# Performance work log

Hardware: AMD Instinct MI355X
Metric: run time of the kernel (lower is better)

## Reference

```python
import jax, jax.numpy as jnp
import numpy as np

B, S, D = 4, 4096, 64
D_MODEL = 64


def setup_inputs() -> dict:
    key = jax.random.key(0)
    kq, kk, kv, km = jax.random.split(key, 4)
    q = jax.random.normal(kq, (B, S, D), dtype=jnp.float32)
    k = jax.random.normal(kk, (B, S, D), dtype=jnp.float32)
    v = jax.random.normal(kv, (B, S, D), dtype=jnp.float32)
    mask = jax.random.uniform(km, (B, S, S), dtype=jnp.float32)
    return {"q": q, "k": k, "v": v, "mask": mask}


def reference(q, k, v, mask):
    dk = jnp.sqrt(jnp.asarray(D_MODEL, dtype=q.dtype))
    # [B,S,S] scores; multiplicative (non-additive) mask applied pre-softmax
    scaled_qk = jnp.einsum('bqd,bkd->bqk', q, k) / dk
    scaled_qk = scaled_qk * mask
    attn = jax.nn.softmax(scaled_qk, axis=-1)
    return jnp.einsum('bqk,bkd->bqd', attn, v)
```

## Files before the change

### kernel.cpp

```cpp
#include <hip/hip_runtime.h>
#include <hip/hip_bf16.h>

#define S_LEN 4096
#define DH 64
#define NBATCH 4

typedef __attribute__((ext_vector_type(8))) short short8;
typedef __attribute__((ext_vector_type(4))) float f32x4;


__global__ __launch_bounds__(256) void cvt_qk_kernel(const float* __restrict__ q,
                                                     const float* __restrict__ k,
                                                     __hip_bfloat16* __restrict__ qb,
                                                     __hip_bfloat16* __restrict__ kb) {
  int i = blockIdx.x * 256 + threadIdx.x;
  qb[i] = __float2bfloat16(q[i]);
  kb[i] = __float2bfloat16(k[i]);
}

__global__ __launch_bounds__(256) void cvt_vT_kernel(const float* __restrict__ v,
                                                     __hip_bfloat16* __restrict__ vt) {
  int i = blockIdx.x * 256 + threadIdx.x;
  int d = i & (DH - 1);
  int s = (i >> 6) & (S_LEN - 1);
  int b = i >> 18;
  vt[(((size_t)b * DH + d) << 12) + s] = __float2bfloat16(v[i]);
}


__global__ __launch_bounds__(256, 4) void fa_kernel(
    const __hip_bfloat16* __restrict__ qb, const __hip_bfloat16* __restrict__ kb,
    const __hip_bfloat16* __restrict__ vt, const float* __restrict__ mask,
    float* __restrict__ out) {
  __shared__ __align__(16) __hip_bfloat16 lds_p[4][16][40];
  __shared__ float lds_O[4][16][64];
  __shared__ float lds_l[4][16];

  const int tid = threadIdx.x;
  const int w = tid >> 6;
  const int lane = tid & 63;
  const int quad = lane >> 4;
  const int n16 = lane & 15;

  const int b = blockIdx.x >> 8;
  const int q0 = (blockIdx.x & 255) << 4;

  const __hip_bfloat16* qrow = qb + (size_t)(b * S_LEN + q0 + n16) * DH;
  const short8 aQ0 = *(const short8*)(qrow + quad * 8);
  const short8 aQ1 = *(const short8*)(qrow + 32 + quad * 8);

  f32x4 O0 = {0.f, 0.f, 0.f, 0.f}, O1 = O0, O2 = O0, O3 = O0;
  float lacc[4] = {0.f, 0.f, 0.f, 0.f};

  const float* mrows[4];
#pragma unroll
  for (int r = 0; r < 4; ++r)
    mrows[r] = mask + ((size_t)b * S_LEN + q0 + quad * 4 + r) * S_LEN;

  const int kstart = w * (S_LEN / 4);
  const __hip_bfloat16* vbase = vt + ((size_t)(b * DH) << 12);

  for (int it = 0; it < (S_LEN / 4) / 32; ++it) {
    const int k0 = kstart + it * 32;

    const __hip_bfloat16* kr0 = kb + (size_t)(b * S_LEN + k0 + n16) * DH;
    const short8 b00 = *(const short8*)(kr0 + quad * 8);
    const short8 b01 = *(const short8*)(kr0 + 32 + quad * 8);
    const short8 b10 = *(const short8*)(kr0 + 16 * DH + quad * 8);
    const short8 b11 = *(const short8*)(kr0 + 16 * DH + 32 + quad * 8);

    const f32x4 z = {0.f, 0.f, 0.f, 0.f};
    f32x4 s0 = __builtin_amdgcn_mfma_f32_16x16x32_bf16(aQ0, b00, z, 0, 0, 0);
    s0 = __builtin_amdgcn_mfma_f32_16x16x32_bf16(aQ1, b01, s0, 0, 0, 0);
    f32x4 s1 = __builtin_amdgcn_mfma_f32_16x16x32_bf16(aQ0, b10, z, 0, 0, 0);
    s1 = __builtin_amdgcn_mfma_f32_16x16x32_bf16(aQ1, b11, s1, 0, 0, 0);

#pragma unroll
    for (int r = 0; r < 4; ++r) {
      float p0 = __expf(s0[r] * 0.125f * mrows[r][k0 + n16]);
      float p1 = __expf(s1[r] * 0.125f * mrows[r][k0 + 16 + n16]);
      lacc[r] += p0 + p1;
      lds_p[w][quad * 4 + r][n16] = __float2bfloat16(p0);
      lds_p[w][quad * 4 + r][16 + n16] = __float2bfloat16(p1);
    }

    const short8 aP = *(const short8*)(&lds_p[w][n16][quad * 8]);

    const __hip_bfloat16* vp = vbase + k0 + quad * 8 + ((size_t)n16 << 12);
    const short8 v0 = *(const short8*)(vp);
    const short8 v1 = *(const short8*)(vp + ((size_t)16 << 12));
    const short8 v2 = *(const short8*)(vp + ((size_t)32 << 12));
    const short8 v3 = *(const short8*)(vp + ((size_t)48 << 12));

    O0 = __builtin_amdgcn_mfma_f32_16x16x32_bf16(aP, v0, O0, 0, 0, 0);
    O1 = __builtin_amdgcn_mfma_f32_16x16x32_bf16(aP, v1, O1, 0, 0, 0);
    O2 = __builtin_amdgcn_mfma_f32_16x16x32_bf16(aP, v2, O2, 0, 0, 0);
    O3 = __builtin_amdgcn_mfma_f32_16x16x32_bf16(aP, v3, O3, 0, 0, 0);
  }

#pragma unroll
  for (int r = 0; r < 4; ++r) {
#pragma unroll
    for (int off = 1; off < 16; off <<= 1) lacc[r] += __shfl_xor(lacc[r], off);
  }

#pragma unroll
  for (int r = 0; r < 4; ++r) {
    int row = quad * 4 + r;
    lds_O[w][row][n16] = O0[r];
    lds_O[w][row][16 + n16] = O1[r];
    lds_O[w][row][32 + n16] = O2[r];
    lds_O[w][row][48 + n16] = O3[r];
    if (n16 == 0) lds_l[w][row] = lacc[r];
  }
  __syncthreads();

  const int r = tid >> 4;
  const int c = (tid & 15) << 2;
  const float linv =
      1.0f / (lds_l[0][r] + lds_l[1][r] + lds_l[2][r] + lds_l[3][r]);
  f32x4 o;
#pragma unroll
  for (int j = 0; j < 4; ++j)
    o[j] = (lds_O[0][r][c + j] + lds_O[1][r][c + j] + lds_O[2][r][c + j] +
            lds_O[3][r][c + j]) *
           linv;
  *(f32x4*)(out + (size_t)(b * S_LEN + q0 + r) * DH + c) = o;
}

extern "C" void kernel_launch(void* const* d_in, const int* in_sizes, int n_in,
                              void* d_out, int out_size, void* d_ws, size_t ws_size,
                              hipStream_t stream) {
  const float* q = (const float*)d_in[0];
  const float* k = (const float*)d_in[1];
  const float* v = (const float*)d_in[2];
  const float* mask = (const float*)d_in[3];
  float* out = (float*)d_out;

  __hip_bfloat16* qb = (__hip_bfloat16*)d_ws;
  __hip_bfloat16* kb = qb + (size_t)NBATCH * S_LEN * DH;
  __hip_bfloat16* vt = kb + (size_t)NBATCH * S_LEN * DH;

  const int nconv_blocks = (NBATCH * S_LEN * DH) / 256;
  cvt_qk_kernel<<<nconv_blocks, 256, 0, stream>>>(q, k, qb, kb);
  cvt_vT_kernel<<<nconv_blocks, 256, 0, stream>>>(v, vt);
  fa_kernel<<<NBATCH * (S_LEN / 16), 256, 0, stream>>>(qb, kb, vt, mask, out);
}
```

Measured before the change: 475.0 us.

## Prefetch mask and K two iterations ahead, interleave warp key ranges, vectorize conversions

The attention kernel now software-pipelines the mask and K fragment loads, using a double-buffered register prefetch that runs two iterations ahead. It also changes the key assignment so the four warps interleave 32-key chunks instead of each owning a contiguous quarter. The Q/K conversion kernel is vectorized to four elements per thread, and the V transpose now goes through a padded LDS tile so that reads and writes are coalesced. These changes aim to hide the latency of the dominant mask stream and to cut prep-kernel overhead, at the cost of more registers per thread.

```diff
diff --git a/kernel.cpp b/kernel.cpp
--- a/kernel.cpp
+++ b/kernel.cpp
@@ -5,34 +5,63 @@
 #define DH 64
 #define NBATCH 4
 
-typedef __attribute__((ext_vector_type(8))) short short8;
+typedef __attribute__((ext_vector_type(8))) short bf16x8;
+typedef __attribute__((ext_vector_type(4))) short bf16x4;
 typedef __attribute__((ext_vector_type(4))) float f32x4;
 
+static __device__ __forceinline__ short f2bf(float x) {
+  __hip_bfloat16 h = __float2bfloat16(x);
+  return *reinterpret_cast<short*>(&h);
+}
+
+#define MFMA(a, b, c) __builtin_amdgcn_mfma_f32_16x16x32_bf16((a), (b), (c), 0, 0, 0)
 
 __global__ __launch_bounds__(256) void cvt_qk_kernel(const float* __restrict__ q,
                                                      const float* __restrict__ k,
-                                                     __hip_bfloat16* __restrict__ qb,
-                                                     __hip_bfloat16* __restrict__ kb) {
-  int i = blockIdx.x * 256 + threadIdx.x;
-  qb[i] = __float2bfloat16(q[i]);
-  kb[i] = __float2bfloat16(k[i]);
+                                                     short* __restrict__ qb,
+                                                     short* __restrict__ kb) {
+  int i = (blockIdx.x * 256 + threadIdx.x) * 4;
+  f32x4 xq = *(const f32x4*)(q + i);
+  f32x4 xk = *(const f32x4*)(k + i);
+  bf16x4 oq, ok;
+#pragma unroll
+  for (int j = 0; j < 4; ++j) { oq[j] = f2bf(xq[j]); ok[j] = f2bf(xk[j]); }
+  *(bf16x4*)(qb + i) = oq;
+  *(bf16x4*)(kb + i) = ok;
 }
 
 __global__ __launch_bounds__(256) void cvt_vT_kernel(const float* __restrict__ v,
-                                                     __hip_bfloat16* __restrict__ vt) {
-  int i = blockIdx.x * 256 + threadIdx.x;
-  int d = i & (DH - 1);
-  int s = (i >> 6) & (S_LEN - 1);
-  int b = i >> 18;
-  vt[(((size_t)b * DH + d) << 12) + s] = __float2bfloat16(v[i]);
+                                                     short* __restrict__ vt) {
+  __shared__ float tile[64][65];
+  const int t = threadIdx.x;
+  const int b = blockIdx.x >> 6;
+  const int s0 = (blockIdx.x & 63) << 6;
+#pragma unroll
+  for (int p = 0; p < 4; ++p) {
+    const int r = p * 16 + (t >> 4);
+    const int c = (t & 15) * 4;
+    const f32x4 x = *(const f32x4*)(v + (size_t)(b * S_LEN + s0 + r) * DH + c);
+    tile[r][c] = x[0]; tile[r][c + 1] = x[1]; tile[r][c + 2] = x[2]; tile[r][c + 3] = x[3];
+  }
+  __syncthreads();
+  const int d = t >> 2;
+  const int sc = (t & 3) * 16;
+  bf16x8 o0, o1;
+#pragma unroll
+  for (int j = 0; j < 8; ++j) {
+    o0[j] = f2bf(tile[sc + j][d]);
+    o1[j] = f2bf(tile[sc + 8 + j][d]);
+  }
+  short* dst = vt + (((size_t)(b * DH + d)) << 12) + s0 + sc;
+  *(bf16x8*)dst = o0;
+  *((bf16x8*)(dst + 8)) = o1;
 }
 
-
 __global__ __launch_bounds__(256, 4) void fa_kernel(
-    const __hip_bfloat16* __restrict__ qb, const __hip_bfloat16* __restrict__ kb,
-    const __hip_bfloat16* __restrict__ vt, const float* __restrict__ mask,
+    const short* __restrict__ qb, const short* __restrict__ kb,
+    const short* __restrict__ vt, const float* __restrict__ mask,
     float* __restrict__ out) {
-  __shared__ __align__(16) __hip_bfloat16 lds_p[4][16][40];
+  __shared__ __align__(16) short lds_p[4][16][40];
   __shared__ float lds_O[4][16][64];
   __shared__ float lds_l[4][16];
 
@@ -45,57 +74,75 @@
   const int b = blockIdx.x >> 8;
   const int q0 = (blockIdx.x & 255) << 4;
 
-  const __hip_bfloat16* qrow = qb + (size_t)(b * S_LEN + q0 + n16) * DH;
-  const short8 aQ0 = *(const short8*)(qrow + quad * 8);
-  const short8 aQ1 = *(const short8*)(qrow + 32 + quad * 8);
+  const short* qrow = qb + (size_t)(b * S_LEN + q0 + n16) * DH;
+  const bf16x8 aQ0 = *(const bf16x8*)(qrow + quad * 8);
+  const bf16x8 aQ1 = *(const bf16x8*)(qrow + 32 + quad * 8);
 
   f32x4 O0 = {0.f, 0.f, 0.f, 0.f}, O1 = O0, O2 = O0, O3 = O0;
   float lacc[4] = {0.f, 0.f, 0.f, 0.f};
 
-  const float* mrows[4];
+  const float* mrow0 = mask + ((size_t)b * S_LEN + q0 + quad * 4) * S_LEN;
+  const short* kbb = kb + (size_t)b * S_LEN * DH;
+  const short* vbase = vt + (((size_t)(b * DH)) << 12);
+
+  float mpf[2][8];
+  bf16x8 kpf[2][4];
+
+  auto load_mask = [&](int k0, float* m) {
 #pragma unroll
-  for (int r = 0; r < 4; ++r)
-    mrows[r] = mask + ((size_t)b * S_LEN + q0 + quad * 4 + r) * S_LEN;
+    for (int r = 0; r < 4; ++r) {
+      m[r]     = mrow0[(size_t)r * S_LEN + k0 + n16];
+      m[4 + r] = mrow0[(size_t)r * S_LEN + k0 + 16 + n16];
+    }
+  };
+  auto load_k = [&](int k0, bf16x8* f) {
+    const short* kr = kbb + (k0 + n16) * DH;
+    f[0] = *(const bf16x8*)(kr + quad * 8);
+    f[1] = *(const bf16x8*)(kr + 32 + quad * 8);
+    f[2] = *(const bf16x8*)(kr + 16 * DH + quad * 8);
+    f[3] = *(const bf16x8*)(kr + 16 * DH + 32 + quad * 8);
+  };
 
-  const int kstart = w * (S_LEN / 4);
-  const __hip_bfloat16* vbase = vt + ((size_t)(b * DH) << 12);
+  load_mask(w * 32, mpf[0]);        load_k(w * 32, kpf[0]);
+  load_mask(128 + w * 32, mpf[1]);  load_k(128 + w * 32, kpf[1]);
 
-  for (int it = 0; it < (S_LEN / 4) / 32; ++it) {
-    const int k0 = kstart + it * 32;
+#pragma unroll 2
+  for (int it = 0; it < 32; ++it) {
+    const int k0 = it * 128 + w * 32;
 
-    const __hip_bfloat16* kr0 = kb + (size_t)(b * S_LEN + k0 + n16) * DH;
-    const short8 b00 = *(const short8*)(kr0 + quad * 8);
-    const short8 b01 = *(const short8*)(kr0 + 32 + quad * 8);
-    const short8 b10 = *(const short8*)(kr0 + 16 * DH + quad * 8);
-    const short8 b11 = *(const short8*)(kr0 + 16 * DH + 32 + quad * 8);
+    float mc[8];
+    bf16x8 bk[4];
+#pragma unroll
+    for (int j = 0; j < 8; ++j) mc[j] = mpf[it & 1][j];
+#pragma unroll
+    for (int j = 0; j < 4; ++j) bk[j] = kpf[it & 1][j];
+    if (it < 30) { load_mask(k0 + 256, mpf[it & 1]); load_k(k0 + 256, kpf[it & 1]); }
+
+    const short* vp = vbase + k0 + quad * 8 + (((size_t)n16) << 12);
+    const bf16x8 v0 = *(const bf16x8*)(vp);
+    const bf16x8 v1 = *(const bf16x8*)(vp + (16 << 12));
+    const bf16x8 v2 = *(const bf16x8*)(vp + (32 << 12));
+    const bf16x8 v3 = *(const bf16x8*)(vp + (48 << 12));
 
     const f32x4 z = {0.f, 0.f, 0.f, 0.f};
-    f32x4 s0 = __builtin_amdgcn_mfma_f32_16x16x32_bf16(aQ0, b00, z, 0, 0, 0);
-    s0 = __builtin_amdgcn_mfma_f32_16x16x32_bf16(aQ1, b01, s0, 0, 0, 0);
-    f32x4 s1 = __builtin_amdgcn_mfma_f32_16x16x32_bf16(aQ0, b10, z, 0, 0, 0);
-    s1 = __builtin_amdgcn_mfma_f32_16x16x32_bf16(aQ1, b11, s1, 0, 0, 0);
+    f32x4 s0 = MFMA(aQ0, bk[0], z); s0 = MFMA(aQ1, bk[1], s0);
+    f32x4 s1 = MFMA(aQ0, bk[2], z); s1 = MFMA(aQ1, bk[3], s1);
 
 #pragma unroll
     for (int r = 0; r < 4; ++r) {
-      float p0 = __expf(s0[r] * 0.125f * mrows[r][k0 + n16]);
-      float p1 = __expf(s1[r] * 0.125f * mrows[r][k0 + 16 + n16]);
+      float p0 = __expf(s0[r] * 0.125f * mc[r]);
+      float p1 = __expf(s1[r] * 0.125f * mc[4 + r]);
       lacc[r] += p0 + p1;
-      lds_p[w][quad * 4 + r][n16] = __float2bfloat16(p0);
-      lds_p[w][quad * 4 + r][16 + n16] = __float2bfloat16(p1);
+      lds_p[w][quad * 4 + r][n16] = f2bf(p0);
+      lds_p[w][quad * 4 + r][16 + n16] = f2bf(p1);
     }
 
-    const short8 aP = *(const short8*)(&lds_p[w][n16][quad * 8]);
+    const bf16x8 aP = *(const bf16x8*)(&lds_p[w][n16][quad * 8]);
 
-    const __hip_bfloat16* vp = vbase + k0 + quad * 8 + ((size_t)n16 << 12);
-    const short8 v0 = *(const short8*)(vp);
-    const short8 v1 = *(const short8*)(vp + ((size_t)16 << 12));
-    const short8 v2 = *(const short8*)(vp + ((size_t)32 << 12));
-    const short8 v3 = *(const short8*)(vp + ((size_t)48 << 12));
-
-    O0 = __builtin_amdgcn_mfma_f32_16x16x32_bf16(aP, v0, O0, 0, 0, 0);
-    O1 = __builtin_amdgcn_mfma_f32_16x16x32_bf16(aP, v1, O1, 0, 0, 0);
-    O2 = __builtin_amdgcn_mfma_f32_16x16x32_bf16(aP, v2, O2, 0, 0, 0);
-    O3 = __builtin_amdgcn_mfma_f32_16x16x32_bf16(aP, v3, O3, 0, 0, 0);
+    O0 = MFMA(aP, v0, O0);
+    O1 = MFMA(aP, v1, O1);
+    O2 = MFMA(aP, v2, O2);
+    O3 = MFMA(aP, v3, O3);
   }
 
 #pragma unroll
@@ -107,7 +154,7 @@
 #pragma unroll
   for (int r = 0; r < 4; ++r) {
     int row = quad * 4 + r;
-    lds_O[w][row][n16] = O0[r];
+    lds_O[w][row][n16]      = O0[r];
     lds_O[w][row][16 + n16] = O1[r];
     lds_O[w][row][32 + n16] = O2[r];
     lds_O[w][row][48 + n16] = O3[r];
@@ -137,12 +184,11 @@
   const float* mask = (const float*)d_in[3];
   float* out = (float*)d_out;
 
-  __hip_bfloat16* qb = (__hip_bfloat16*)d_ws;
-  __hip_bfloat16* kb = qb + (size_t)NBATCH * S_LEN * DH;
-  __hip_bfloat16* vt = kb + (size_t)NBATCH * S_LEN * DH;
+  short* qb = (short*)d_ws;
+  short* kb = qb + (size_t)NBATCH * S_LEN * DH;
+  short* vt = kb + (size_t)NBATCH * S_LEN * DH;
 
-  const int nconv_blocks = (NBATCH * S_LEN * DH) / 256;
-  cvt_qk_kernel<<<nconv_blocks, 256, 0, stream>>>(q, k, qb, kb);
-  cvt_vT_kernel<<<nconv_blocks, 256, 0, stream>>>(v, vt);
+  cvt_qk_kernel<<<(NBATCH * S_LEN * DH) / (256 * 4), 256, 0, stream>>>(q, k, qb, kb);
+  cvt_vT_kernel<<<NBATCH * (S_LEN / 64), 256, 0, stream>>>(v, vt);
   fa_kernel<<<NBATCH * (S_LEN / 16), 256, 0, stream>>>(qb, kb, vt, mask, out);
 }
```

New measurement: 520.5 us. 1.1x slower.
